# Kernel optimization log

Measured on AMD Instinct MI355X. Metric: run time of the kernel, lower is better.

## Reference

```python
import jax, jax.numpy as jnp
import numpy as np

HEADS = 4

def _conv1x1(x, w, b):
    # 1x1 conv == channel-mixing matmul; w: [C_out, C_in], b: [C_out]
    return jnp.einsum('bchw,oc->bohw', x, w) + b[None, :, None, None]

def setup_inputs() -> dict:
    key = jax.random.key(0)
    ks = jax.random.split(key, 9)
    B, C, H, W = 4, 64, 64, 64
    x = jax.random.normal(ks[0], (B, C, H, W), dtype=jnp.float32)
    scale = 0.05
    wq = jax.random.normal(ks[1], (C, C), dtype=jnp.float32) * scale
    bq = jax.random.normal(ks[2], (C,), dtype=jnp.float32) * scale
    wk = jax.random.normal(ks[3], (C, C), dtype=jnp.float32) * scale
    bk = jax.random.normal(ks[4], (C,), dtype=jnp.float32) * scale
    wv = jax.random.normal(ks[5], (C, C), dtype=jnp.float32) * scale
    bv = jax.random.normal(ks[6], (C,), dtype=jnp.float32) * scale
    wp = jax.random.normal(ks[7], (C, C), dtype=jnp.float32) * scale
    bp = jax.random.normal(ks[8], (C,), dtype=jnp.float32) * scale
    return {"x": x, "wq": wq, "bq": bq, "wk": wk, "bk": bk,
            "wv": wv, "bv": bv, "wp": wp, "bp": bp}

def reference(x, wq, bq, wk, bk, wv, bv, wp, bp):
    B, C, H, W = x.shape
    HW = H * W
    ch = C // HEADS  # head dim
    q = _conv1x1(x, wq, bq).reshape(B, HEADS, ch, HW)
    k = _conv1x1(x, wk, bk).reshape(B, HEADS, ch, HW)
    v = _conv1x1(x, wv, bv).reshape(B, HEADS, ch, HW)
    # scores[b,h,i,j] = sum_c q[b,h,c,i] * k[b,h,c,j]  -> [B, H, HW, HW]
    scores = jnp.einsum('bhci,bhcj->bhij', q, k)
    attn = jax.nn.softmax(scores, axis=-1)
    # out: [B, heads, HW, ch]
    out = jnp.einsum('bhij,bhcj->bhic', attn, v)
    # faithful to torch .view: raw contiguous reshape (NOT a transpose back)
    out = out.reshape(B, C, H, W)
    return _conv1x1(out, wp, bp)
```

## Files before the change

kernel.cpp:

```cpp
#include <hip/hip_runtime.h>

#define LOG2E 1.4426950408889634f


using s8v   = __attribute__((ext_vector_type(8))) short;
using u16x8 = __attribute__((ext_vector_type(8))) unsigned short;
using f32x4 = __attribute__((ext_vector_type(4))) float;

static __device__ __forceinline__ unsigned short bf16b(float f) {
  return __builtin_bit_cast(unsigned short, (__bf16)f);
}

__global__ __launch_bounds__(256) void qkv_proj(
    const float* __restrict__ x,
    const float* __restrict__ wq, const float* __restrict__ bq,
    const float* __restrict__ wk, const float* __restrict__ bk,
    const float* __restrict__ wv, const float* __restrict__ bv,
    float* __restrict__ qb, unsigned short* __restrict__ kT,
    unsigned short* __restrict__ vb) {
  __shared__ __align__(16) float xs[64][64];
  __shared__ float wqs[64][65];
  __shared__ float wks[64][65];
  __shared__ float wvs[64][65];
  int t = threadIdx.x;
  int b = blockIdx.x >> 6;
  int px0 = (blockIdx.x & 63) << 6;
#pragma unroll
  for (int kk = 0; kk < 16; kk++) {
    int idx = kk * 256 + t;
    int c = idx >> 6, px = idx & 63;
    xs[c][px] = x[((size_t)(b * 64 + c) << 12) + px0 + px];
    int o = idx >> 6, c2 = idx & 63;
    wqs[c2][o] = wq[idx];
    wks[c2][o] = wk[idx];
    wvs[c2][o] = wv[idx];
  }
  __syncthreads();

  int o = t & 63;
  int pw = (t >> 6) << 4;
  float aq[16], ak[16], av[16];
#pragma unroll
  for (int p = 0; p < 16; p++) { aq[p] = 0.f; ak[p] = 0.f; av[p] = 0.f; }

  for (int c = 0; c < 64; c++) {
    float wqv = wqs[c][o], wkv = wks[c][o], wvv = wvs[c][o];
    float xr[16];
#pragma unroll
    for (int g = 0; g < 4; g++) {
      float4 x4 = *reinterpret_cast<const float4*>(&xs[c][pw + 4 * g]);
      xr[4 * g] = x4.x; xr[4 * g + 1] = x4.y; xr[4 * g + 2] = x4.z; xr[4 * g + 3] = x4.w;
    }
#pragma unroll
    for (int p = 0; p < 16; p++) {
      aq[p] += wqv * xr[p];
      ak[p] += wkv * xr[p];
      av[p] += wvv * xr[p];
    }
  }

  float bqv = bq[o], bkv = bk[o], bvv = bv[o];
  {
    float* dstq = qb + ((size_t)(b * 64 + o) << 12) + px0 + pw;
#pragma unroll
    for (int g = 0; g < 4; g++) {
      float4 q4 = { (aq[4 * g + 0] + bqv) * LOG2E, (aq[4 * g + 1] + bqv) * LOG2E,
                    (aq[4 * g + 2] + bqv) * LOG2E, (aq[4 * g + 3] + bqv) * LOG2E };
      reinterpret_cast<float4*>(dstq)[g] = q4;
    }
    unsigned short* dstv = vb + ((size_t)(b * 64 + o) << 12) + px0 + pw;
    u16x8 v0, v1;
#pragma unroll
    for (int p = 0; p < 8; p++) {
      v0[p] = bf16b(av[p] + bvv);
      v1[p] = bf16b(av[8 + p] + bvv);
    }
    *reinterpret_cast<u16x8*>(dstv) = v0;
    *reinterpret_cast<u16x8*>(dstv + 8) = v1;
  }
  int bh = b * 4 + (o >> 4);
  int chn = o & 15;
  size_t kb = ((size_t)bh << 16) + ((size_t)(px0 + pw) << 4) + chn;
#pragma unroll
  for (int p = 0; p < 16; p++) {
    kT[kb + ((size_t)p << 4)] = bf16b(ak[p] + bkv);
  }
}

__global__ __launch_bounds__(256) void attn_mfma(
    const float* __restrict__ qb, const unsigned short* __restrict__ kT,
    const unsigned short* __restrict__ vb, float* __restrict__ ao) {
  __shared__ float red[4][64][18];
  const int tid  = threadIdx.x;
  const int w    = tid >> 6;
  const int lane = tid & 63;
  const int i_   = lane & 15;
  const int q4   = lane >> 4;
  const int chb  = (q4 & 1) << 3;

  const int orig = ((blockIdx.x & 7) << 7) + (blockIdx.x >> 3);
  const int bh = orig >> 6;
  const int i0 = (orig & 63) << 6;
  const int b = bh >> 2, h = bh & 3;

  s8v BQ[4];
#pragma unroll
  for (int g = 0; g < 4; ++g) {
    const float* qp = qb + (((size_t)(b * 64 + h * 16 + chb)) << 12) + (i0 + (g << 4) + i_);
#pragma unroll
    for (int e = 0; e < 8; ++e) {
      float f = qp[(size_t)e << 12];
      __bf16 hi = (__bf16)f;
      float v = (q4 < 2) ? (float)hi : (f - (float)hi);
      BQ[g][e] = __builtin_bit_cast(short, (__bf16)v);
    }
  }

  f32x4 acc[4];
  float l[4];
#pragma unroll
  for (int g = 0; g < 4; ++g) {
    acc[g] = (f32x4){0.f, 0.f, 0.f, 0.f};
    l[g] = 0.f;
  }

  const unsigned short* vpb = vb + (((size_t)(b * 64 + h * 16 + i_)) << 12);
  const unsigned short* kpb = kT + ((size_t)bh << 16);

  for (int t = 0; t < 32; ++t) {
    const int jb = (w << 10) + (t << 5);
    s8v AV;
    {
      struct { uint2 a, b; } pair;
      pair.a = *(const uint2*)(vpb + jb + (q4 << 2));
      pair.b = *(const uint2*)(vpb + jb + 16 + (q4 << 2));
      AV = __builtin_bit_cast(s8v, pair);
    }
    s8v AK0 = *(const s8v*)(kpb + (((size_t)(jb + i_)) << 4) + chb);
    s8v AK1 = *(const s8v*)(kpb + (((size_t)(jb + 16 + i_)) << 4) + chb);

#pragma unroll
    for (int g = 0; g < 4; ++g) {
      f32x4 z = {0.f, 0.f, 0.f, 0.f};
      f32x4 s0 = __builtin_amdgcn_mfma_f32_16x16x32_bf16(AK0, BQ[g], z, 0, 0, 0);
      f32x4 s1 = __builtin_amdgcn_mfma_f32_16x16x32_bf16(AK1, BQ[g], z, 0, 0, 0);
      float p0 = __builtin_amdgcn_exp2f(s0[0]);
      float p1 = __builtin_amdgcn_exp2f(s0[1]);
      float p2 = __builtin_amdgcn_exp2f(s0[2]);
      float p3 = __builtin_amdgcn_exp2f(s0[3]);
      float p4 = __builtin_amdgcn_exp2f(s1[0]);
      float p5 = __builtin_amdgcn_exp2f(s1[1]);
      float p6 = __builtin_amdgcn_exp2f(s1[2]);
      float p7 = __builtin_amdgcn_exp2f(s1[3]);
      l[g] += (((p0 + p1) + (p2 + p3)) + ((p4 + p5) + (p6 + p7)));
      s8v PB;
      PB[0] = (short)bf16b(p0); PB[1] = (short)bf16b(p1);
      PB[2] = (short)bf16b(p2); PB[3] = (short)bf16b(p3);
      PB[4] = (short)bf16b(p4); PB[5] = (short)bf16b(p5);
      PB[6] = (short)bf16b(p6); PB[7] = (short)bf16b(p7);
      acc[g] = __builtin_amdgcn_mfma_f32_16x16x32_bf16(AV, PB, acc[g], 0, 0, 0);
    }
  }

#pragma unroll
  for (int g = 0; g < 4; ++g) {
    float lg = l[g];
    lg += __shfl_xor(lg, 16);
    lg += __shfl_xor(lg, 32);
    int iq = (g << 4) + i_;
    if (q4 == 0) red[w][iq][0] = lg;
    red[w][iq][1 + (q4 << 2) + 0] = acc[g][0];
    red[w][iq][1 + (q4 << 2) + 1] = acc[g][1];
    red[w][iq][1 + (q4 << 2) + 2] = acc[g][2];
    red[w][iq][1 + (q4 << 2) + 3] = acc[g][3];
  }
  __syncthreads();

  {
    int iq = tid & 63, quad = tid >> 6;
    float L = (red[0][iq][0] + red[1][iq][0]) + (red[2][iq][0] + red[3][iq][0]);
    float o0 = 0.f, o1 = 0.f, o2 = 0.f, o3 = 0.f;
#pragma unroll
    for (int s = 0; s < 4; ++s) {
      o0 += red[s][iq][1 + (quad << 2) + 0];
      o1 += red[s][iq][1 + (quad << 2) + 1];
      o2 += red[s][iq][1 + (quad << 2) + 2];
      o3 += red[s][iq][1 + (quad << 2) + 3];
    }
    float inv = 1.0f / L;
    float4 o = { o0 * inv, o1 * inv, o2 * inv, o3 * inv };
    *(float4*)&ao[((((size_t)bh << 12) + i0 + iq) << 4) + (quad << 2)] = o;
  }
}

__global__ __launch_bounds__(256) void out_proj(
    const float* __restrict__ a, const float* __restrict__ wp,
    const float* __restrict__ bp, float* __restrict__ out) {
  __shared__ __align__(16) float as[64][64];
  __shared__ float wps[64][65];
  int t = threadIdx.x;
  int b = blockIdx.x >> 6;
  int px0 = (blockIdx.x & 63) << 6;
#pragma unroll
  for (int kk = 0; kk < 16; kk++) {
    int idx = kk * 256 + t;
    int c = idx >> 6, px = idx & 63;
    as[c][px] = a[((size_t)b << 18) + ((size_t)c << 12) + px0 + px];
    int o = idx >> 6, c2 = idx & 63;
    wps[c2][o] = wp[idx];
  }
  __syncthreads();

  int o = t & 63;
  int pw = (t >> 6) << 4;
  float acc[16];
#pragma unroll
  for (int p = 0; p < 16; p++) acc[p] = 0.f;
  for (int c = 0; c < 64; c++) {
    float wv = wps[c][o];
    float xr[16];
#pragma unroll
    for (int g = 0; g < 4; g++) {
      float4 x4 = *reinterpret_cast<const float4*>(&as[c][pw + 4 * g]);
      xr[4 * g] = x4.x; xr[4 * g + 1] = x4.y; xr[4 * g + 2] = x4.z; xr[4 * g + 3] = x4.w;
    }
#pragma unroll
    for (int p = 0; p < 16; p++) acc[p] += wv * xr[p];
  }
  float bv = bp[o];
  float* dst = out + ((size_t)(b * 64 + o) << 12) + px0 + pw;
#pragma unroll
  for (int g = 0; g < 4; g++) {
    float4 v4 = { acc[4 * g + 0] + bv, acc[4 * g + 1] + bv,
                  acc[4 * g + 2] + bv, acc[4 * g + 3] + bv };
    reinterpret_cast<float4*>(dst)[g] = v4;
  }
}

extern "C" void kernel_launch(void* const* d_in, const int* in_sizes, int n_in,
                              void* d_out, int out_size, void* d_ws, size_t ws_size,
                              hipStream_t stream) {
  (void)in_sizes; (void)n_in; (void)out_size; (void)ws_size;
  const float* x  = (const float*)d_in[0];
  const float* wq = (const float*)d_in[1];
  const float* bq = (const float*)d_in[2];
  const float* wk = (const float*)d_in[3];
  const float* bk = (const float*)d_in[4];
  const float* wv = (const float*)d_in[5];
  const float* bv = (const float*)d_in[6];
  const float* wp = (const float*)d_in[7];
  const float* bp = (const float*)d_in[8];

  float* ws = (float*)d_ws;
  float* qb = ws;
  unsigned short* kT = (unsigned short*)(ws + (1u << 20));
  unsigned short* vT = (unsigned short*)(ws + (1u << 20) + (1u << 19));
  float* ao = ws + 2u * (1u << 20);

  qkv_proj<<<256, 256, 0, stream>>>(x, wq, bq, wk, bk, wv, bv, qb, kT, vT);
  attn_mfma<<<1024, 256, 0, stream>>>(qb, kT, vT, ao);
  out_proj<<<256, 256, 0, stream>>>(ao, wp, bp, (float*)d_out);
}
```

Before: 71.83 us.

## Transpose Q layout, prefetch K/V tiles, compute softmax denominator via MFMA

The Q projection is now stored transposed, matching the K layout, so the attention kernel loads each Q fragment with two float4 reads instead of eight strided scalar loads. The K/V fragment loads are software-pipelined one iteration ahead to hide global-memory latency behind the MFMA and exp work. The softmax row sum is moved from VALU adds plus cross-lane shuffles into an extra MFMA against a vector of bf16 ones. In exchange the row sum now accumulates bf16-rounded probabilities, there is one extra MFMA per group, register pressure rises from the prefetch buffers, and the qkv_proj Q stores become strided scalar writes.

Result: slower. 77.50 us (+7.9%).

```diff
diff --git a/kernel.cpp b/kernel.cpp
--- a/kernel.cpp
+++ b/kernel.cpp
@@ -16,7 +16,7 @@
     const float* __restrict__ wq, const float* __restrict__ bq,
     const float* __restrict__ wk, const float* __restrict__ bk,
     const float* __restrict__ wv, const float* __restrict__ bv,
-    float* __restrict__ qb, unsigned short* __restrict__ kT,
+    float* __restrict__ qT, unsigned short* __restrict__ kT,
     unsigned short* __restrict__ vb) {
   __shared__ __align__(16) float xs[64][64];
   __shared__ float wqs[64][65];
@@ -61,13 +61,6 @@
 
   float bqv = bq[o], bkv = bk[o], bvv = bv[o];
   {
-    float* dstq = qb + ((size_t)(b * 64 + o) << 12) + px0 + pw;
-#pragma unroll
-    for (int g = 0; g < 4; g++) {
-      float4 q4 = { (aq[4 * g + 0] + bqv) * LOG2E, (aq[4 * g + 1] + bqv) * LOG2E,
-                    (aq[4 * g + 2] + bqv) * LOG2E, (aq[4 * g + 3] + bqv) * LOG2E };
-      reinterpret_cast<float4*>(dstq)[g] = q4;
-    }
     unsigned short* dstv = vb + ((size_t)(b * 64 + o) << 12) + px0 + pw;
     u16x8 v0, v1;
 #pragma unroll
@@ -83,12 +76,13 @@
   size_t kb = ((size_t)bh << 16) + ((size_t)(px0 + pw) << 4) + chn;
 #pragma unroll
   for (int p = 0; p < 16; p++) {
+    qT[kb + ((size_t)p << 4)] = (aq[p] + bqv) * LOG2E;
     kT[kb + ((size_t)p << 4)] = bf16b(ak[p] + bkv);
   }
 }
 
 __global__ __launch_bounds__(256) void attn_mfma(
-    const float* __restrict__ qb, const unsigned short* __restrict__ kT,
+    const float* __restrict__ qT, const unsigned short* __restrict__ kT,
     const unsigned short* __restrict__ vb, float* __restrict__ ao) {
   __shared__ float red[4][64][18];
   const int tid  = threadIdx.x;
@@ -106,38 +100,55 @@
   s8v BQ[4];
 #pragma unroll
   for (int g = 0; g < 4; ++g) {
-    const float* qp = qb + (((size_t)(b * 64 + h * 16 + chb)) << 12) + (i0 + (g << 4) + i_);
+    const float* qp = qT + ((size_t)bh << 16) + ((size_t)(i0 + (g << 4) + i_) << 4) + chb;
+    float4 f0 = *(const float4*)qp;
+    float4 f1 = *(const float4*)(qp + 4);
+    float fr[8] = { f0.x, f0.y, f0.z, f0.w, f1.x, f1.y, f1.z, f1.w };
 #pragma unroll
     for (int e = 0; e < 8; ++e) {
-      float f = qp[(size_t)e << 12];
+      float f = fr[e];
       __bf16 hi = (__bf16)f;
       float v = (q4 < 2) ? (float)hi : (f - (float)hi);
       BQ[g][e] = __builtin_bit_cast(short, (__bf16)v);
     }
   }
 
-  f32x4 acc[4];
-  float l[4];
+  s8v ones;
+#pragma unroll
+  for (int e = 0; e < 8; ++e) ones[e] = (short)0x3F80;
+
+  f32x4 acc[4], accl[4];
 #pragma unroll
   for (int g = 0; g < 4; ++g) {
     acc[g] = (f32x4){0.f, 0.f, 0.f, 0.f};
-    l[g] = 0.f;
+    accl[g] = (f32x4){0.f, 0.f, 0.f, 0.f};
   }
 
   const unsigned short* vpb = vb + (((size_t)(b * 64 + h * 16 + i_)) << 12);
   const unsigned short* kpb = kT + ((size_t)bh << 16);
 
+  s8v AV, AK0, AK1;
+  {
+    const int jb = (w << 10);
+    struct { uint2 a, b; } pair;
+    pair.a = *(const uint2*)(vpb + jb + (q4 << 2));
+    pair.b = *(const uint2*)(vpb + jb + 16 + (q4 << 2));
+    AV = __builtin_bit_cast(s8v, pair);
+    AK0 = *(const s8v*)(kpb + (((size_t)(jb + i_)) << 4) + chb);
+    AK1 = *(const s8v*)(kpb + (((size_t)(jb + 16 + i_)) << 4) + chb);
+  }
+
   for (int t = 0; t < 32; ++t) {
-    const int jb = (w << 10) + (t << 5);
-    s8v AV;
+    s8v nAV, nAK0, nAK1;
     {
+      const int jn = (w << 10) + (((t + 1) & 31) << 5);
       struct { uint2 a, b; } pair;
-      pair.a = *(const uint2*)(vpb + jb + (q4 << 2));
-      pair.b = *(const uint2*)(vpb + jb + 16 + (q4 << 2));
-      AV = __builtin_bit_cast(s8v, pair);
-    }
-    s8v AK0 = *(const s8v*)(kpb + (((size_t)(jb + i_)) << 4) + chb);
-    s8v AK1 = *(const s8v*)(kpb + (((size_t)(jb + 16 + i_)) << 4) + chb);
+      pair.a = *(const uint2*)(vpb + jn + (q4 << 2));
+      pair.b = *(const uint2*)(vpb + jn + 16 + (q4 << 2));
+      nAV = __builtin_bit_cast(s8v, pair);
+      nAK0 = *(const s8v*)(kpb + (((size_t)(jn + i_)) << 4) + chb);
+      nAK1 = *(const s8v*)(kpb + (((size_t)(jn + 16 + i_)) << 4) + chb);
+    }
 
 #pragma unroll
     for (int g = 0; g < 4; ++g) {
@@ -152,23 +163,21 @@
       float p5 = __builtin_amdgcn_exp2f(s1[1]);
       float p6 = __builtin_amdgcn_exp2f(s1[2]);
       float p7 = __builtin_amdgcn_exp2f(s1[3]);
-      l[g] += (((p0 + p1) + (p2 + p3)) + ((p4 + p5) + (p6 + p7)));
       s8v PB;
       PB[0] = (short)bf16b(p0); PB[1] = (short)bf16b(p1);
       PB[2] = (short)bf16b(p2); PB[3] = (short)bf16b(p3);
       PB[4] = (short)bf16b(p4); PB[5] = (short)bf16b(p5);
       PB[6] = (short)bf16b(p6); PB[7] = (short)bf16b(p7);
-      acc[g] = __builtin_amdgcn_mfma_f32_16x16x32_bf16(AV, PB, acc[g], 0, 0, 0);
-    }
+      acc[g]  = __builtin_amdgcn_mfma_f32_16x16x32_bf16(AV, PB, acc[g], 0, 0, 0);
+      accl[g] = __builtin_amdgcn_mfma_f32_16x16x32_bf16(ones, PB, accl[g], 0, 0, 0);
+    }
+    AV = nAV; AK0 = nAK0; AK1 = nAK1;
   }
 
 #pragma unroll
   for (int g = 0; g < 4; ++g) {
-    float lg = l[g];
-    lg += __shfl_xor(lg, 16);
-    lg += __shfl_xor(lg, 32);
     int iq = (g << 4) + i_;
-    if (q4 == 0) red[w][iq][0] = lg;
+    if (q4 == 0) red[w][iq][0] = accl[g][0];
     red[w][iq][1 + (q4 << 2) + 0] = acc[g][0];
     red[w][iq][1 + (q4 << 2) + 1] = acc[g][1];
     red[w][iq][1 + (q4 << 2) + 2] = acc[g][2];
@@ -252,12 +261,12 @@
   const float* bp = (const float*)d_in[8];
 
   float* ws = (float*)d_ws;
-  float* qb = ws;
+  float* qT = ws;
   unsigned short* kT = (unsigned short*)(ws + (1u << 20));
   unsigned short* vT = (unsigned short*)(ws + (1u << 20) + (1u << 19));
   float* ao = ws + 2u * (1u << 20);
 
-  qkv_proj<<<256, 256, 0, stream>>>(x, wq, bq, wk, bk, wv, bv, qb, kT, vT);
-  attn_mfma<<<1024, 256, 0, stream>>>(qb, kT, vT, ao);
+  qkv_proj<<<256, 256, 0, stream>>>(x, wq, bq, wk, bk, wv, bv, qT, kT, vT);
+  attn_mfma<<<1024, 256, 0, stream>>>(qT, kT, vT, ao);
   out_proj<<<256, 256, 0, stream>>>(ao, wp, bp, (float*)d_out);
 }
```
